# Kernel optimization log

Hardware: AMD Instinct MI355X
Metric: run time of the kernel (lower is better)

The kernel has to match this reference:

```python
import jax, jax.numpy as jnp
import numpy as np

SIZES = [64, 64, 64, 64]
N_SAMPLES = 8192


def radialkernel(u, v):
    # exp(u.v^T - |u|^2/2 - |v|^2/2), shape [rows(u), rows(v)]
    uu = jnp.sum(u * u, axis=1, keepdims=True)
    vv = jnp.sum(v * v, axis=1, keepdims=True)
    return jnp.exp(u @ v.T - uu / 2 - vv.T / 2)


def setup_inputs() -> dict:
    key = jax.random.key(0)
    k0, k1, k2, k3 = jax.random.split(key, 4)
    d_in = 256
    total = sum(SIZES)            # 256
    rest = sum(SIZES[1:])         # 192
    data = jax.random.normal(k0, (N_SAMPLES, d_in), jnp.float32)
    inputs = jax.random.normal(k1, (2048, d_in), jnp.float32)
    # Linear(d_in, total): weight [total, d_in], bias [total]
    W = jax.random.normal(k2, (total, d_in), jnp.float32) / np.sqrt(d_in)
    b = jnp.zeros((total,), jnp.float32)
    # xavier_uniform for c_ss [N, rest]
    limit = np.sqrt(6.0 / (N_SAMPLES + rest)).astype(np.float32)
    c_ss = jax.random.uniform(k3, (N_SAMPLES, rest), jnp.float32, -limit, limit)
    return {"data": data, "inputs": inputs, "W": W, "b": b, "c_ss": c_ss}


def reference(data, inputs, W, b, c_ss):
    n = N_SAMPLES
    x = jnp.concatenate([data, inputs], axis=0) @ W.T + b  # [N+B, total]
    reg = jnp.sum(W * W) + jnp.sum(b * b)
    xss = list(jnp.split(x, np.cumsum(SIZES[:-1]), axis=1))
    css = jnp.split(c_ss, np.cumsum(SIZES[1:-1]), axis=1)
    ker = jnp.zeros((x.shape[0], n), x.dtype)
    for i, cs in enumerate(css):  # len(sizes)-1 iterations (small, fixed)
        xs = xss[i]
        ker = ker + radialkernel(xs, xs[:n])  # [N+B, N]
        val = ker @ cs                        # [N+B, sizes[i+1]]
        xss[i + 1] = xss[i + 1] + val
        reg = reg + jnp.sum(cs * val[:n])
    return xss[-1][n:], reg
```

## Files before the change

kernel.cpp:

```cpp
#include <hip/hip_runtime.h>
#include <hip/hip_bf16.h>

typedef unsigned short u16;
typedef unsigned int   u32;
typedef __attribute__((ext_vector_type(8)))  short bf16x8;
typedef __attribute__((ext_vector_type(16))) float f32x16;

#define N_S   8192
#define M_TOT 10240
#define SEGS  8
#define SEG   1024
#define QT    320

__device__ __forceinline__ u16 f2bf(float f) {
  u32 x = __float_as_uint(f);
  u32 r = x + 0x7FFFu + ((x >> 16) & 1u);
  return (u16)(r >> 16);
}
__device__ __forceinline__ float bf2f(u16 h) {
  return __uint_as_float(((u32)h) << 16);
}

__global__ __launch_bounds__(256) void gemm_x(const float* __restrict__ data,
                                              const float* __restrict__ inp,
                                              const float* __restrict__ W,
                                              const float* __restrict__ bias,
                                              float* __restrict__ x,
                                              u16* __restrict__ xb0,
                                              u32* __restrict__ hl0)
{
  __shared__ __align__(16) u16 At[64 * 256];
  __shared__ __align__(16) u16 Wt[64 * 256];
  __shared__ float part[64][2];
  const int t  = threadIdx.x;
  const int rb = blockIdx.x * 64, cb = blockIdx.y * 64;
  if (cb == 192 && rb + 64 <= N_S) return;

#pragma unroll
  for (int it = 0; it < 8; ++it) {
    int c = it * 256 + t;
    int row = c >> 5, c8 = c & 31;
    int grow = rb + row;
    const float* src = (grow < N_S) ? data + (size_t)grow * 256 + c8 * 8
                                    : inp + (size_t)(grow - N_S) * 256 + c8 * 8;
    float4 v0 = *(const float4*)src;
    float4 v1 = *(const float4*)(src + 4);
    u16 h[8] = {f2bf(v0.x), f2bf(v0.y), f2bf(v0.z), f2bf(v0.w),
                f2bf(v1.x), f2bf(v1.y), f2bf(v1.z), f2bf(v1.w)};
    *(int4*)((char*)At + row * 512 + ((c8 * 16) ^ ((row & 7) << 4))) = *(int4*)h;

    const float* wsrc = W + (size_t)(cb + row) * 256 + c8 * 8;
    float4 w0 = *(const float4*)wsrc;
    float4 w1 = *(const float4*)(wsrc + 4);
    u16 g[8] = {f2bf(w0.x), f2bf(w0.y), f2bf(w0.z), f2bf(w0.w),
                f2bf(w1.x), f2bf(w1.y), f2bf(w1.z), f2bf(w1.w)};
    *(int4*)((char*)Wt + row * 512 + ((c8 * 16) ^ ((row & 7) << 4))) = *(int4*)g;
  }
  __syncthreads();

  const int w = t >> 6, lane = t & 63, l31 = lane & 31, hi = lane >> 5;
  const int wr = (w >> 1) * 32, wc = (w & 1) * 32;
  f32x16 acc;
#pragma unroll
  for (int r = 0; r < 16; ++r) acc[r] = 0.f;
  const char* Ab = (const char*)At + (size_t)(wr + l31) * 512;
  const char* Bb = (const char*)Wt + (size_t)(wc + l31) * 512;
  const int rx = (l31 & 7) << 4;
#pragma unroll
  for (int k0 = 0; k0 < 256; k0 += 16) {
    bf16x8 af = *(const bf16x8*)(Ab + ((k0 * 2 + hi * 16) ^ rx));
    bf16x8 bfv = *(const bf16x8*)(Bb + ((k0 * 2 + hi * 16) ^ rx));
    acc = __builtin_amdgcn_mfma_f32_32x32x16_bf16(af, bfv, acc, 0, 0, 0);
  }
  float bv = bias[cb + wc + l31];
#pragma unroll
  for (int r = 0; r < 16; ++r) {
    int qr = (r & 3) + 8 * (r >> 2) + 4 * hi;
    x[(size_t)(rb + wr + qr) * 256 + cb + wc + l31] = acc[r] + bv;
  }

  if (cb == 0) {
#pragma unroll
    for (int r = 0; r < 16; ++r) {
      int qr = (r & 3) + 8 * (r >> 2) + 4 * hi;
      u16 h = f2bf(acc[r] + bv);
      xb0[(size_t)(rb + wr + qr) * 64 + wc + l31] = h;
      float fb = bf2f(h);
      float s = fb * fb;
      s += __shfl_xor(s, 1);
      s += __shfl_xor(s, 2);
      s += __shfl_xor(s, 4);
      s += __shfl_xor(s, 8);
      s += __shfl_xor(s, 16);
      if (l31 == 0) part[wr + qr][w & 1] = s;
    }
    __syncthreads();
    if (t < 64) {
      float A = 0.5f * (part[t][0] + part[t][1]);
      u16 hq = f2bf(A);
      u16 lq = f2bf(A - bf2f(hq));
      hl0[rb + t] = (u32)hq | ((u32)lq << 16);
    }
  }
}

__global__ __launch_bounds__(256) void setup_ker(const float* __restrict__ css,
                                                 const float* __restrict__ W,
                                                 const float* __restrict__ bias,
                                                 u16* __restrict__ csbT,
                                                 float* __restrict__ regpart,
                                                 u32* __restrict__ mask,
                                                 u32* __restrict__ counter)
{
  __shared__ float tile[64][65];
  __shared__ float red[256];
  const int b = blockIdx.x, t = threadIdx.x;
  if (b < 384) {
    const int i  = b >> 7;
    const int r0 = (b & 127) * 64;
#pragma unroll
    for (int it = 0; it < 4; ++it) {
      int r  = (t >> 4) + it * 16;
      int c4 = (t & 15) * 4;
      float4 v = *(const float4*)(css + (size_t)(r0 + r) * 192 + i * 64 + c4);
      tile[r][c4] = v.x; tile[r][c4 + 1] = v.y; tile[r][c4 + 2] = v.z; tile[r][c4 + 3] = v.w;
    }
    __syncthreads();
    const int c = t >> 2, rq = (t & 3) * 16;
    u16 tmp[16];
#pragma unroll
    for (int e = 0; e < 16; ++e) tmp[e] = f2bf(tile[rq + e][c]);
    u16* dst = csbT + (size_t)i * (64 * (size_t)N_S) + (size_t)c * N_S + r0 + rq;
    *(int4*)dst       = *(int4*)tmp;
    *(int4*)(dst + 8) = *(int4*)(tmp + 8);
  } else {
    const int b2 = b - 384;
    const int gid = b2 * 256 + t;
    if (gid < 3 * QT * SEGS) mask[gid] = 0u;
    if (gid == 0) *counter = 0u;
    float4 v = *(const float4*)(W + (size_t)b2 * 1024 + t * 4);
    float s = v.x * v.x + v.y * v.y + v.z * v.z + v.w * v.w;
    if (b2 == 0) { float bv = bias[t]; s += bv * bv; }
    red[t] = s; __syncthreads();
#pragma unroll
    for (int o = 128; o; o >>= 1) {
      if (t < o) red[t] += red[t + o];
      __syncthreads();
    }
    if (t == 0) regpart[b2] = red[0];
  }
}

__global__ __launch_bounds__(64) void screen_ker(const u16* __restrict__ xbj,
                                                 const u32* __restrict__ hlj,
                                                 u32* __restrict__ maskj)
{
  const int qq  = blockIdx.x;
  const int seg = blockIdx.y;
  const int w   = blockIdx.z;
  const int nt0 = seg * 32 + w * 4;
  if (qq < 64 && qq * 4 + 3 < nt0) return;

  const int lane = threadIdx.x & 63, l31 = lane & 31, hi = lane >> 5;

  bf16x8 qf[4][4];
  u32 hlq[4];
#pragma unroll
  for (int q = 0; q < 4; ++q) {
    const int qrow = (qq * 4 + q) * 32 + l31;
    const u16* qp = xbj + (size_t)qrow * 64 + hi * 8;
#pragma unroll
    for (int d = 0; d < 4; ++d) qf[q][d] = *(const bf16x8*)(qp + d * 16);
    hlq[q] = hlj[qrow];
  }

  f32x16 Z;
#pragma unroll
  for (int r = 0; r < 16; ++r) Z[r] = 0.f;

  u32 bits[4] = {0u, 0u, 0u, 0u};
#pragma unroll
  for (int it = 0; it < 4; ++it) {
    const int kt = nt0 + it;
    const int nb = kt * 32;
    const u16* kp = xbj + (size_t)(nb + l31) * 64 + hi * 8;
    bf16x8 kf0 = *(const bf16x8*)(kp);
    bf16x8 kf1 = *(const bf16x8*)(kp + 16);
    bf16x8 kf2 = *(const bf16x8*)(kp + 32);
    bf16x8 kf3 = *(const bf16x8*)(kp + 48);
    u32 hlk = hlj[nb + l31];
    union { bf16x8 v; u32 d[4]; } ke;
    ke.d[0] = hi ? 0u : 0xBF80BF80u;
    ke.d[1] = hi ? 0u : (hlk ^ 0x80008000u);
    ke.d[2] = 0u; ke.d[3] = 0u;
#pragma unroll
    for (int q = 0; q < 4; ++q) {
      f32x16 S = __builtin_amdgcn_mfma_f32_32x32x16_bf16(qf[q][0], kf0, Z, 0, 0, 0);
      S = __builtin_amdgcn_mfma_f32_32x32x16_bf16(qf[q][1], kf1, S, 0, 0, 0);
      S = __builtin_amdgcn_mfma_f32_32x32x16_bf16(qf[q][2], kf2, S, 0, 0, 0);
      S = __builtin_amdgcn_mfma_f32_32x32x16_bf16(qf[q][3], kf3, S, 0, 0, 0);
      union { bf16x8 v; u32 d[4]; } qe;
      qe.d[0] = hi ? 0u : hlq[q];
      qe.d[1] = hi ? 0u : 0x3F803F80u;
      qe.d[2] = 0u; qe.d[3] = 0u;
      S = __builtin_amdgcn_mfma_f32_32x32x16_bf16(qe.v, ke.v, S, 0, 0, 0);
      float m0 = fmaxf(S[0], S[1]),  m1 = fmaxf(S[2], S[3]);
      float m2 = fmaxf(S[4], S[5]),  m3 = fmaxf(S[6], S[7]);
      float m4 = fmaxf(S[8], S[9]),  m5 = fmaxf(S[10], S[11]);
      float m6 = fmaxf(S[12], S[13]), m7 = fmaxf(S[14], S[15]);
      float mx = fmaxf(fmaxf(fmaxf(m0, m1), fmaxf(m2, m3)),
                       fmaxf(fmaxf(m4, m5), fmaxf(m6, m7)));
      bool act = __any(mx > -25.0f) != 0;
      bits[q] |= (act ? 1u : 0u) << it;
      const int qtile = qq * 4 + q;
      if (act && qtile < 256 && kt < qtile && lane == 0)
        atomicOr(&maskj[(size_t)kt * SEGS + (qtile >> 5)], 1u << (qtile & 31));
    }
  }
  if (lane == 0) {
#pragma unroll
    for (int q = 0; q < 4; ++q)
      if (bits[q]) atomicOr(&maskj[(size_t)(qq * 4 + q) * SEGS + seg], bits[q] << (w * 4));
  }
}

template<int NJ>
__global__ __launch_bounds__(256) void fa_ker(const u16* __restrict__ xb,
                                              const u32* __restrict__ hl,
                                              const u16* __restrict__ csbT,
                                              const u32* __restrict__ mask,
                                              const float* __restrict__ css,
                                              float* __restrict__ x,
                                              float* __restrict__ dotpart,
                                              u16* __restrict__ xbn,
                                              u32* __restrict__ hln,
                                              float* __restrict__ out,
                                              const float* __restrict__ regpart,
                                              u32* __restrict__ counter)
{
  __shared__ __align__(16) u16 Pt[4][32 * 32];
  __shared__ float accs[4][32][64];
  __shared__ float red[256];
  __shared__ int lastFlag;

  const int t    = threadIdx.x;
  const int w    = t >> 6;
  const int lane = t & 63;
  const int l31  = lane & 31;
  const int hi   = lane >> 5;
  const int qtile = blockIdx.x;
  const int qrow  = qtile * 32 + l31;
  constexpr int I = NJ - 1;

  bf16x8 qf[NJ][4];
  u32    hlq[NJ];
#pragma unroll
  for (int j = 0; j < NJ; ++j) {
    const u16* xbj = xb + (size_t)j * ((size_t)M_TOT * 64);
#pragma unroll
    for (int dk = 0; dk < 4; ++dk)
      qf[j][dk] = *(const bf16x8*)(xbj + (size_t)qrow * 64 + dk * 16 + hi * 8);
    hlq[j] = hl[j * M_TOT + qrow];
  }

  f32x16 acc0, acc1;
#pragma unroll
  for (int r = 0; r < 16; ++r) { acc0[r] = 0.f; acc1[r] = 0.f; }

  int idx = 0;
  for (int seg = 0; seg < SEGS; ++seg) {
    u32 mj[NJ];
    u32 uni = 0;
#pragma unroll
    for (int j = 0; j < NJ; ++j) {
      mj[j] = mask[((size_t)j * QT + qtile) * SEGS + seg];
      uni |= mj[j];
    }
    u32 rem = uni;
    while (rem) {
      const int nt = __ffs(rem) - 1;
      rem &= rem - 1;
      if ((idx++ & 3) != w) continue;
      const int nb = seg * SEG + nt * 32;
      f32x16 P;
#pragma unroll
      for (int r = 0; r < 16; ++r) P[r] = 0.f;
#pragma unroll
      for (int j = 0; j < NJ; ++j) {
        if ((mj[j] >> nt) & 1u) {
          const u16* xbj = xb + (size_t)j * ((size_t)M_TOT * 64);
          const u16* kp = xbj + (size_t)(nb + l31) * 64 + hi * 8;
          bf16x8 kf0 = *(const bf16x8*)(kp);
          bf16x8 kf1 = *(const bf16x8*)(kp + 16);
          bf16x8 kf2 = *(const bf16x8*)(kp + 32);
          bf16x8 kf3 = *(const bf16x8*)(kp + 48);
          u32 hlk = hl[j * M_TOT + nb + l31];
          f32x16 S;
#pragma unroll
          for (int r = 0; r < 16; ++r) S[r] = 0.f;
          S = __builtin_amdgcn_mfma_f32_32x32x16_bf16(qf[j][0], kf0, S, 0, 0, 0);
          S = __builtin_amdgcn_mfma_f32_32x32x16_bf16(qf[j][1], kf1, S, 0, 0, 0);
          S = __builtin_amdgcn_mfma_f32_32x32x16_bf16(qf[j][2], kf2, S, 0, 0, 0);
          S = __builtin_amdgcn_mfma_f32_32x32x16_bf16(qf[j][3], kf3, S, 0, 0, 0);
          union { bf16x8 v; u32 d[4]; } qe, ke;
          qe.d[0] = hi ? 0u : hlq[j];
          qe.d[1] = hi ? 0u : 0x3F803F80u;
          qe.d[2] = 0u; qe.d[3] = 0u;
          ke.d[0] = hi ? 0u : 0xBF80BF80u;
          ke.d[1] = hi ? 0u : (hlk ^ 0x80008000u);
          ke.d[2] = 0u; ke.d[3] = 0u;
          S = __builtin_amdgcn_mfma_f32_32x32x16_bf16(qe.v, ke.v, S, 0, 0, 0);
#pragma unroll
          for (int r = 0; r < 16; ++r) P[r] += __expf(S[r]);
        }
      }
      char* pw = (char*)&Pt[w][0];
#pragma unroll
      for (int r = 0; r < 16; ++r) {
        int qr = (r & 3) + 8 * (r >> 2) + 4 * hi;
        *(u16*)(pw + qr * 64 + ((l31 * 2) ^ ((qr & 3) << 4))) = f2bf(P[r]);
      }
      asm volatile("s_waitcnt lgkmcnt(0)" ::: "memory");
      bf16x8 pa0 = *(const bf16x8*)(pw + l31 * 64 + ((0  + hi * 16) ^ ((l31 & 3) << 4)));
      bf16x8 pa1 = *(const bf16x8*)(pw + l31 * 64 + ((32 + hi * 16) ^ ((l31 & 3) << 4)));
      asm volatile("s_waitcnt lgkmcnt(0)" ::: "memory");
      bf16x8 v00 = *(const bf16x8*)(csbT + (size_t)l31 * N_S + nb + hi * 8);
      bf16x8 v01 = *(const bf16x8*)(csbT + (size_t)l31 * N_S + nb + 16 + hi * 8);
      bf16x8 v10 = *(const bf16x8*)(csbT + (size_t)(32 + l31) * N_S + nb + hi * 8);
      bf16x8 v11 = *(const bf16x8*)(csbT + (size_t)(32 + l31) * N_S + nb + 16 + hi * 8);
      acc0 = __builtin_amdgcn_mfma_f32_32x32x16_bf16(pa0, v00, acc0, 0, 0, 0);
      acc0 = __builtin_amdgcn_mfma_f32_32x32x16_bf16(pa1, v01, acc0, 0, 0, 0);
      acc1 = __builtin_amdgcn_mfma_f32_32x32x16_bf16(pa0, v10, acc1, 0, 0, 0);
      acc1 = __builtin_amdgcn_mfma_f32_32x32x16_bf16(pa1, v11, acc1, 0, 0, 0);
    }
  }

#pragma unroll
  for (int r = 0; r < 16; ++r) {
    int qr = (r & 3) + 8 * (r >> 2) + 4 * hi;
    accs[w][qr][l31]      = acc0[r];
    accs[w][qr][32 + l31] = acc1[r];
  }
  __syncthreads();

  const int rr   = t >> 3;
  const int row  = qtile * 32 + rr;
  const int coff = (t & 7) * 8;
  float v[8];
#pragma unroll
  for (int e = 0; e < 8; ++e)
    v[e] = ((accs[0][rr][coff + e] + accs[1][rr][coff + e]) +
            (accs[2][rr][coff + e] + accs[3][rr][coff + e]));

  float dp = 0.f;
  if (row < N_S) {
    const float* cp = css + (size_t)row * 192 + (size_t)I * 64 + coff;
    float4 ca = *(const float4*)cp;
    float4 cb = *(const float4*)(cp + 4);
    dp = ca.x * v[0] + ca.y * v[1] + ca.z * v[2] + ca.w * v[3]
       + cb.x * v[4] + cb.y * v[5] + cb.z * v[6] + cb.w * v[7];
  }

  if (NJ < 3) {
    float* xp = x + (size_t)row * 256 + (size_t)(I + 1) * 64 + coff;
    float4 xa = *(const float4*)xp;
    float4 xb4 = *(const float4*)(xp + 4);
    xa.x += v[0]; xa.y += v[1]; xa.z += v[2]; xa.w += v[3];
    xb4.x += v[4]; xb4.y += v[5]; xb4.z += v[6]; xb4.w += v[7];
    *(float4*)xp = xa;
    *(float4*)(xp + 4) = xb4;
    float xv[8] = {xa.x, xa.y, xa.z, xa.w, xb4.x, xb4.y, xb4.z, xb4.w};
    u16 h[8];
    float s2 = 0.f;
#pragma unroll
    for (int e = 0; e < 8; ++e) {
      h[e] = f2bf(xv[e]);
      float fb = bf2f(h[e]);
      s2 += fb * fb;
    }
    *(int4*)(xbn + (size_t)row * 64 + coff) = *(int4*)h;
    s2 += __shfl_xor(s2, 1);
    s2 += __shfl_xor(s2, 2);
    s2 += __shfl_xor(s2, 4);
    if ((t & 7) == 0) {
      float A = 0.5f * s2;
      u16 hq = f2bf(A);
      u16 lq = f2bf(A - bf2f(hq));
      hln[row] = (u32)hq | ((u32)lq << 16);
    }
  } else if (row >= N_S) {
    const float* xp = x + (size_t)row * 256 + 192 + coff;
    float4 xa = *(const float4*)xp;
    float4 xb4 = *(const float4*)(xp + 4);
    float* op = out + (size_t)(row - N_S) * 64 + coff;
    float4 oa = {xa.x + v[0], xa.y + v[1], xa.z + v[2], xa.w + v[3]};
    float4 ob = {xb4.x + v[4], xb4.y + v[5], xb4.z + v[6], xb4.w + v[7]};
    *(float4*)op = oa;
    *(float4*)(op + 4) = ob;
  }

  red[t] = dp; __syncthreads();
#pragma unroll
  for (int o = 128; o; o >>= 1) {
    if (t < o) red[t] += red[t + o];
    __syncthreads();
  }
  if (t == 0) dotpart[I * QT + qtile] = red[0];

  if (NJ == 3) {
    if (t == 0) {
      u32 c = __hip_atomic_fetch_add(counter, 1u, __ATOMIC_ACQ_REL, __HIP_MEMORY_SCOPE_AGENT);
      lastFlag = (c == QT - 1) ? 1 : 0;
    }
    __syncthreads();
    if (lastFlag) {
      float s = 0.f;
      for (int i2 = t; i2 < 3 * QT; i2 += 256) s += dotpart[i2];
      if (t < 64) s += regpart[t];
      red[t] = s; __syncthreads();
#pragma unroll
      for (int o = 128; o; o >>= 1) {
        if (t < o) red[t] += red[t + o];
        __syncthreads();
      }
      if (t == 0) out[131072] = red[0];
    }
  }
}

extern "C" void kernel_launch(void* const* d_in, const int* in_sizes, int n_in,
                              void* d_out, int out_size, void* d_ws, size_t ws_size,
                              hipStream_t stream)
{
  const float* data = (const float*)d_in[0];
  const float* inp  = (const float*)d_in[1];
  const float* W    = (const float*)d_in[2];
  const float* bias = (const float*)d_in[3];
  const float* css  = (const float*)d_in[4];
  float* out = (float*)d_out;

  char* ws = (char*)d_ws;
  const size_t OFF_X    = 0;
  const size_t OFF_XB   = 10485760;
  const size_t OFF_HL   = OFF_XB + 3932160;
  const size_t OFF_CSBT = OFF_HL + 122880;
  const size_t OFF_MASK = OFF_CSBT + 3145728;
  const size_t OFF_REGW = OFF_MASK + 30720;
  const size_t OFF_DOT  = OFF_REGW + 256;
  const size_t OFF_CNT  = OFF_DOT + 3840;

  float* x      = (float*)(ws + OFF_X);
  u16*   xb     = (u16*)  (ws + OFF_XB);
  u32*   hl     = (u32*)  (ws + OFF_HL);
  u16*   csbT   = (u16*)  (ws + OFF_CSBT);
  u32*   mask   = (u32*)  (ws + OFF_MASK);
  float* regpart= (float*)(ws + OFF_REGW);
  float* dotpart= (float*)(ws + OFF_DOT);
  u32*   counter= (u32*)  (ws + OFF_CNT);

  const size_t XB_STRIDE = (size_t)M_TOT * 64;
  const size_t CS_STRIDE = (size_t)64 * N_S;
  const size_t MK_STRIDE = (size_t)QT * SEGS;

  setup_ker<<<448, 256, 0, stream>>>(css, W, bias, csbT, regpart, mask, counter);
  gemm_x   <<<dim3(160, 4), 256, 0, stream>>>(data, inp, W, bias, x, xb, hl);
  screen_ker<<<dim3(80, SEGS, 8), 64, 0, stream>>>(xb, hl, mask);

  fa_ker<1><<<QT, 256, 0, stream>>>(xb, hl, csbT, mask, css, x, dotpart,
                                    xb + XB_STRIDE, hl + M_TOT, (float*)nullptr,
                                    regpart, counter);
  screen_ker<<<dim3(80, SEGS, 8), 64, 0, stream>>>(xb + XB_STRIDE, hl + M_TOT, mask + MK_STRIDE);

  fa_ker<2><<<QT, 256, 0, stream>>>(xb, hl, csbT + CS_STRIDE, mask, css, x, dotpart,
                                    xb + 2 * XB_STRIDE, hl + 2 * M_TOT, (float*)nullptr,
                                    regpart, counter);
  screen_ker<<<dim3(80, SEGS, 8), 64, 0, stream>>>(xb + 2 * XB_STRIDE, hl + 2 * M_TOT, mask + 2 * MK_STRIDE);

  fa_ker<3><<<QT, 256, 0, stream>>>(xb, hl, csbT + 2 * CS_STRIDE, mask, css, x, dotpart,
                                    (u16*)nullptr, (u32*)nullptr, out,
                                    regpart, counter);
}
```

Baseline: 134.5 us.

## Fuse setup into projection GEMM and skip empty query tiles in attention

Merges the setup kernel (transposing c_ss to bf16, zeroing the mask, reducing the weight norms) into the projection GEMM as extra blocks, so one launch replaces two. The GEMM now also writes the bf16 copy and half-norms for column blocks 1 and 2. This lets each fa_ker block whose screening masks are all empty skip the query loads, the kernel accumulation and the x/xbn update entirely. The cost is a larger shared-memory footprint per GEMM block and extra bf16 stores that run even for tiles that do real work.

```diff
diff --git a/kernel.cpp b/kernel.cpp
--- a/kernel.cpp
+++ b/kernel.cpp
@@ -21,20 +21,70 @@
   return __uint_as_float(((u32)h) << 16);
 }
 
-__global__ __launch_bounds__(256) void gemm_x(const float* __restrict__ data,
-                                              const float* __restrict__ inp,
-                                              const float* __restrict__ W,
-                                              const float* __restrict__ bias,
-                                              float* __restrict__ x,
-                                              u16* __restrict__ xb0,
-                                              u32* __restrict__ hl0)
+__global__ __launch_bounds__(256) void gemm_setup(const float* __restrict__ data,
+                                                  const float* __restrict__ inp,
+                                                  const float* __restrict__ W,
+                                                  const float* __restrict__ bias,
+                                                  const float* __restrict__ css,
+                                                  float* __restrict__ x,
+                                                  u16* __restrict__ xb,
+                                                  u32* __restrict__ hl,
+                                                  u16* __restrict__ csbT,
+                                                  float* __restrict__ regpart,
+                                                  u32* __restrict__ mask,
+                                                  u32* __restrict__ counter)
 {
-  __shared__ __align__(16) u16 At[64 * 256];
-  __shared__ __align__(16) u16 Wt[64 * 256];
-  __shared__ float part[64][2];
-  const int t  = threadIdx.x;
-  const int rb = blockIdx.x * 64, cb = blockIdx.y * 64;
+  __shared__ __align__(16) char smem[66048];
+  const int b = blockIdx.x, t = threadIdx.x;
+
+  if (b >= 640) {
+    const int bs = b - 640;
+    if (bs < 384) {
+      float (*tile)[65] = (float(*)[65])smem;
+      const int i  = bs >> 7;
+      const int r0 = (bs & 127) * 64;
+#pragma unroll
+      for (int it = 0; it < 4; ++it) {
+        int r  = (t >> 4) + it * 16;
+        int c4 = (t & 15) * 4;
+        float4 v = *(const float4*)(css + (size_t)(r0 + r) * 192 + i * 64 + c4);
+        tile[r][c4] = v.x; tile[r][c4 + 1] = v.y; tile[r][c4 + 2] = v.z; tile[r][c4 + 3] = v.w;
+      }
+      __syncthreads();
+      const int c = t >> 2, rq = (t & 3) * 16;
+      u16 tmp[16];
+#pragma unroll
+      for (int e = 0; e < 16; ++e) tmp[e] = f2bf(tile[rq + e][c]);
+      u16* dst = csbT + (size_t)i * (64 * (size_t)N_S) + (size_t)c * N_S + r0 + rq;
+      *(int4*)dst       = *(int4*)tmp;
+      *(int4*)(dst + 8) = *(int4*)(tmp + 8);
+    } else {
+      float* red = (float*)smem;
+      const int b2 = bs - 384;
+      const int gid = b2 * 256 + t;
+      if (gid < 3 * QT * SEGS) mask[gid] = 0u;
+      if (gid == 0) *counter = 0u;
+      float4 v = *(const float4*)(W + (size_t)b2 * 1024 + t * 4);
+      float s = v.x * v.x + v.y * v.y + v.z * v.z + v.w * v.w;
+      if (b2 == 0) { float bv = bias[t]; s += bv * bv; }
+      red[t] = s; __syncthreads();
+#pragma unroll
+      for (int o = 128; o; o >>= 1) {
+        if (t < o) red[t] += red[t + o];
+        __syncthreads();
+      }
+      if (t == 0) regpart[b2] = red[0];
+    }
+    return;
+  }
+
+  const int rowblk = b >> 2, cbi = b & 3;
+  const int rb = rowblk * 64, cb = cbi * 64;
   if (cb == 192 && rb + 64 <= N_S) return;
+
+  u16* At = (u16*)smem;
+  u16* Wt = (u16*)(smem + 32768);
+  float (*part)[2] = (float(*)[2])(smem + 65536);
 
 #pragma unroll
   for (int it = 0; it < 8; ++it) {
@@ -79,12 +129,14 @@
     x[(size_t)(rb + wr + qr) * 256 + cb + wc + l31] = acc[r] + bv;
   }
 
-  if (cb == 0) {
+  if (cb < 192) {
+    u16* xbc = xb + (size_t)cbi * ((size_t)M_TOT * 64);
+    u32* hlc = hl + (size_t)cbi * M_TOT;
 #pragma unroll
     for (int r = 0; r < 16; ++r) {
       int qr = (r & 3) + 8 * (r >> 2) + 4 * hi;
       u16 h = f2bf(acc[r] + bv);
-      xb0[(size_t)(rb + wr + qr) * 64 + wc + l31] = h;
+      xbc[(size_t)(rb + wr + qr) * 64 + wc + l31] = h;
       float fb = bf2f(h);
       float s = fb * fb;
       s += __shfl_xor(s, 1);
@@ -99,55 +151,8 @@
       float A = 0.5f * (part[t][0] + part[t][1]);
       u16 hq = f2bf(A);
       u16 lq = f2bf(A - bf2f(hq));
-      hl0[rb + t] = (u32)hq | ((u32)lq << 16);
-    }
-  }
-}
-
-__global__ __launch_bounds__(256) void setup_ker(const float* __restrict__ css,
-                                                 const float* __restrict__ W,
-                                                 const float* __restrict__ bias,
-                                                 u16* __restrict__ csbT,
-                                                 float* __restrict__ regpart,
-                                                 u32* __restrict__ mask,
-                                                 u32* __restrict__ counter)
-{
-  __shared__ float tile[64][65];
-  __shared__ float red[256];
-  const int b = blockIdx.x, t = threadIdx.x;
-  if (b < 384) {
-    const int i  = b >> 7;
-    const int r0 = (b & 127) * 64;
-#pragma unroll
-    for (int it = 0; it < 4; ++it) {
-      int r  = (t >> 4) + it * 16;
-      int c4 = (t & 15) * 4;
-      float4 v = *(const float4*)(css + (size_t)(r0 + r) * 192 + i * 64 + c4);
-      tile[r][c4] = v.x; tile[r][c4 + 1] = v.y; tile[r][c4 + 2] = v.z; tile[r][c4 + 3] = v.w;
-    }
-    __syncthreads();
-    const int c = t >> 2, rq = (t & 3) * 16;
-    u16 tmp[16];
-#pragma unroll
-    for (int e = 0; e < 16; ++e) tmp[e] = f2bf(tile[rq + e][c]);
-    u16* dst = csbT + (size_t)i * (64 * (size_t)N_S) + (size_t)c * N_S + r0 + rq;
-    *(int4*)dst       = *(int4*)tmp;
-    *(int4*)(dst + 8) = *(int4*)(tmp + 8);
-  } else {
-    const int b2 = b - 384;
-    const int gid = b2 * 256 + t;
-    if (gid < 3 * QT * SEGS) mask[gid] = 0u;
-    if (gid == 0) *counter = 0u;
-    float4 v = *(const float4*)(W + (size_t)b2 * 1024 + t * 4);
-    float s = v.x * v.x + v.y * v.y + v.z * v.z + v.w * v.w;
-    if (b2 == 0) { float bv = bias[t]; s += bv * bv; }
-    red[t] = s; __syncthreads();
-#pragma unroll
-    for (int o = 128; o; o >>= 1) {
-      if (t < o) red[t] += red[t + o];
-      __syncthreads();
-    }
-    if (t == 0) regpart[b2] = red[0];
+      hlc[rb + t] = (u32)hq | ((u32)lq << 16);
+    }
   }
 }
 
@@ -252,141 +257,157 @@
   const int qrow  = qtile * 32 + l31;
   constexpr int I = NJ - 1;
 
-  bf16x8 qf[NJ][4];
-  u32    hlq[NJ];
-#pragma unroll
-  for (int j = 0; j < NJ; ++j) {
-    const u16* xbj = xb + (size_t)j * ((size_t)M_TOT * 64);
-#pragma unroll
-    for (int dk = 0; dk < 4; ++dk)
-      qf[j][dk] = *(const bf16x8*)(xbj + (size_t)qrow * 64 + dk * 16 + hi * 8);
-    hlq[j] = hl[j * M_TOT + qrow];
-  }
-
-  f32x16 acc0, acc1;
-#pragma unroll
-  for (int r = 0; r < 16; ++r) { acc0[r] = 0.f; acc1[r] = 0.f; }
-
-  int idx = 0;
+  u32 mj_all[NJ][SEGS];
+  u32 uni_s[SEGS];
+  u32 anyu = 0;
+#pragma unroll
   for (int seg = 0; seg < SEGS; ++seg) {
-    u32 mj[NJ];
-    u32 uni = 0;
+    u32 u = 0;
 #pragma unroll
     for (int j = 0; j < NJ; ++j) {
-      mj[j] = mask[((size_t)j * QT + qtile) * SEGS + seg];
-      uni |= mj[j];
-    }
-    u32 rem = uni;
-    while (rem) {
-      const int nt = __ffs(rem) - 1;
-      rem &= rem - 1;
-      if ((idx++ & 3) != w) continue;
-      const int nb = seg * SEG + nt * 32;
-      f32x16 P;
-#pragma unroll
-      for (int r = 0; r < 16; ++r) P[r] = 0.f;
-#pragma unroll
-      for (int j = 0; j < NJ; ++j) {
-        if ((mj[j] >> nt) & 1u) {
-          const u16* xbj = xb + (size_t)j * ((size_t)M_TOT * 64);
-          const u16* kp = xbj + (size_t)(nb + l31) * 64 + hi * 8;
-          bf16x8 kf0 = *(const bf16x8*)(kp);
-          bf16x8 kf1 = *(const bf16x8*)(kp + 16);
-          bf16x8 kf2 = *(const bf16x8*)(kp + 32);
-          bf16x8 kf3 = *(const bf16x8*)(kp + 48);
-          u32 hlk = hl[j * M_TOT + nb + l31];
-          f32x16 S;
-#pragma unroll
-          for (int r = 0; r < 16; ++r) S[r] = 0.f;
-          S = __builtin_amdgcn_mfma_f32_32x32x16_bf16(qf[j][0], kf0, S, 0, 0, 0);
-          S = __builtin_amdgcn_mfma_f32_32x32x16_bf16(qf[j][1], kf1, S, 0, 0, 0);
-          S = __builtin_amdgcn_mfma_f32_32x32x16_bf16(qf[j][2], kf2, S, 0, 0, 0);
-          S = __builtin_amdgcn_mfma_f32_32x32x16_bf16(qf[j][3], kf3, S, 0, 0, 0);
-          union { bf16x8 v; u32 d[4]; } qe, ke;
-          qe.d[0] = hi ? 0u : hlq[j];
-          qe.d[1] = hi ? 0u : 0x3F803F80u;
-          qe.d[2] = 0u; qe.d[3] = 0u;
-          ke.d[0] = hi ? 0u : 0xBF80BF80u;
-          ke.d[1] = hi ? 0u : (hlk ^ 0x80008000u);
-          ke.d[2] = 0u; ke.d[3] = 0u;
-          S = __builtin_amdgcn_mfma_f32_32x32x16_bf16(qe.v, ke.v, S, 0, 0, 0);
-#pragma unroll
-          for (int r = 0; r < 16; ++r) P[r] += __expf(S[r]);
+      mj_all[j][seg] = mask[((size_t)j * QT + qtile) * SEGS + seg];
+      u |= mj_all[j][seg];
+    }
+    uni_s[seg] = u;
+    anyu |= u;
+  }
+
+  if (anyu) {
+    bf16x8 qf[NJ][4];
+    u32    hlq[NJ];
+#pragma unroll
+    for (int j = 0; j < NJ; ++j) {
+      const u16* xbj = xb + (size_t)j * ((size_t)M_TOT * 64);
+#pragma unroll
+      for (int dk = 0; dk < 4; ++dk)
+        qf[j][dk] = *(const bf16x8*)(xbj + (size_t)qrow * 64 + dk * 16 + hi * 8);
+      hlq[j] = hl[j * M_TOT + qrow];
+    }
+
+    f32x16 acc0, acc1;
+#pragma unroll
+    for (int r = 0; r < 16; ++r) { acc0[r] = 0.f; acc1[r] = 0.f; }
+
+    int idx = 0;
+    for (int seg = 0; seg < SEGS; ++seg) {
+      u32 rem = uni_s[seg];
+      while (rem) {
+        const int nt = __ffs(rem) - 1;
+        rem &= rem - 1;
+        if ((idx++ & 3) != w) continue;
+        const int nb = seg * SEG + nt * 32;
+        f32x16 P;
+#pragma unroll
+        for (int r = 0; r < 16; ++r) P[r] = 0.f;
+#pragma unroll
+        for (int j = 0; j < NJ; ++j) {
+          if ((mj_all[j][seg] >> nt) & 1u) {
+            const u16* xbj = xb + (size_t)j * ((size_t)M_TOT * 64);
+            const u16* kp = xbj + (size_t)(nb + l31) * 64 + hi * 8;
+            bf16x8 kf0 = *(const bf16x8*)(kp);
+            bf16x8 kf1 = *(const bf16x8*)(kp + 16);
+            bf16x8 kf2 = *(const bf16x8*)(kp + 32);
+            bf16x8 kf3 = *(const bf16x8*)(kp + 48);
+            u32 hlk = hl[j * M_TOT + nb + l31];
+            f32x16 S;
+#pragma unroll
+            for (int r = 0; r < 16; ++r) S[r] = 0.f;
+            S = __builtin_amdgcn_mfma_f32_32x32x16_bf16(qf[j][0], kf0, S, 0, 0, 0);
+            S = __builtin_amdgcn_mfma_f32_32x32x16_bf16(qf[j][1], kf1, S, 0, 0, 0);
+            S = __builtin_amdgcn_mfma_f32_32x32x16_bf16(qf[j][2], kf2, S, 0, 0, 0);
+            S = __builtin_amdgcn_mfma_f32_32x32x16_bf16(qf[j][3], kf3, S, 0, 0, 0);
+            union { bf16x8 v; u32 d[4]; } qe, ke;
+            qe.d[0] = hi ? 0u : hlq[j];
+            qe.d[1] = hi ? 0u : 0x3F803F80u;
+            qe.d[2] = 0u; qe.d[3] = 0u;
+            ke.d[0] = hi ? 0u : 0xBF80BF80u;
+            ke.d[1] = hi ? 0u : (hlk ^ 0x80008000u);
+            ke.d[2] = 0u; ke.d[3] = 0u;
+            S = __builtin_amdgcn_mfma_f32_32x32x16_bf16(qe.v, ke.v, S, 0, 0, 0);
+#pragma unroll
+            for (int r = 0; r < 16; ++r) P[r] += __expf(S[r]);
+          }
         }
+        char* pw = (char*)&Pt[w][0];
+#pragma unroll
+        for (int r = 0; r < 16; ++r) {
+          int qr = (r & 3) + 8 * (r >> 2) + 4 * hi;
+          *(u16*)(pw + qr * 64 + ((l31 * 2) ^ ((qr & 3) << 4))) = f2bf(P[r]);
+        }
+        asm volatile("s_waitcnt lgkmcnt(0)" ::: "memory");
+        bf16x8 pa0 = *(const bf16x8*)(pw + l31 * 64 + ((0  + hi * 16) ^ ((l31 & 3) << 4)));
+        bf16x8 pa1 = *(const bf16x8*)(pw + l31 * 64 + ((32 + hi * 16) ^ ((l31 & 3) << 4)));
+        asm volatile("s_waitcnt lgkmcnt(0)" ::: "memory");
+        bf16x8 v00 = *(const bf16x8*)(csbT + (size_t)l31 * N_S + nb + hi * 8);
+        bf16x8 v01 = *(const bf16x8*)(csbT + (size_t)l31 * N_S + nb + 16 + hi * 8);
+        bf16x8 v10 = *(const bf16x8*)(csbT + (size_t)(32 + l31) * N_S + nb + hi * 8);
+        bf16x8 v11 = *(const bf16x8*)(csbT + (size_t)(32 + l31) * N_S + nb + 16 + hi * 8);
+        acc0 = __builtin_amdgcn_mfma_f32_32x32x16_bf16(pa0, v00, acc0, 0, 0, 0);
+        acc0 = __builtin_amdgcn_mfma_f32_32x32x16_bf16(pa1, v01, acc0, 0, 0, 0);
+        acc1 = __builtin_amdgcn_mfma_f32_32x32x16_bf16(pa0, v10, acc1, 0, 0, 0);
+        acc1 = __builtin_amdgcn_mfma_f32_32x32x16_bf16(pa1, v11, acc1, 0, 0, 0);
       }
-      char* pw = (char*)&Pt[w][0];
-#pragma unroll
-      for (int r = 0; r < 16; ++r) {
-        int qr = (r & 3) + 8 * (r >> 2) + 4 * hi;
-        *(u16*)(pw + qr * 64 + ((l31 * 2) ^ ((qr & 3) << 4))) = f2bf(P[r]);
-      }
-      asm volatile("s_waitcnt lgkmcnt(0)" ::: "memory");
-      bf16x8 pa0 = *(const bf16x8*)(pw + l31 * 64 + ((0  + hi * 16) ^ ((l31 & 3) << 4)));
-      bf16x8 pa1 = *(const bf16x8*)(pw + l31 * 64 + ((32 + hi * 16) ^ ((l31 & 3) << 4)));
-      asm volatile("s_waitcnt lgkmcnt(0)" ::: "memory");
-      bf16x8 v00 = *(const bf16x8*)(csbT + (size_t)l31 * N_S + nb + hi * 8);
-      bf16x8 v01 = *(const bf16x8*)(csbT + (size_t)l31 * N_S + nb + 16 + hi * 8);
-      bf16x8 v10 = *(const bf16x8*)(csbT + (size_t)(32 + l31) * N_S + nb + hi * 8);
-      bf16x8 v11 = *(const bf16x8*)(csbT + (size_t)(32 + l31) * N_S + nb + 16 + hi * 8);
-      acc0 = __builtin_amdgcn_mfma_f32_32x32x16_bf16(pa0, v00, acc0, 0, 0, 0);
-      acc0 = __builtin_amdgcn_mfma_f32_32x32x16_bf16(pa1, v01, acc0, 0, 0, 0);
-      acc1 = __builtin_amdgcn_mfma_f32_32x32x16_bf16(pa0, v10, acc1, 0, 0, 0);
-      acc1 = __builtin_amdgcn_mfma_f32_32x32x16_bf16(pa1, v11, acc1, 0, 0, 0);
-    }
-  }
-
-#pragma unroll
-  for (int r = 0; r < 16; ++r) {
-    int qr = (r & 3) + 8 * (r >> 2) + 4 * hi;
-    accs[w][qr][l31]      = acc0[r];
-    accs[w][qr][32 + l31] = acc1[r];
-  }
-  __syncthreads();
+    }
+
+#pragma unroll
+    for (int r = 0; r < 16; ++r) {
+      int qr = (r & 3) + 8 * (r >> 2) + 4 * hi;
+      accs[w][qr][l31]      = acc0[r];
+      accs[w][qr][32 + l31] = acc1[r];
+    }
+    __syncthreads();
+  }
 
   const int rr   = t >> 3;
   const int row  = qtile * 32 + rr;
   const int coff = (t & 7) * 8;
   float v[8];
 #pragma unroll
-  for (int e = 0; e < 8; ++e)
-    v[e] = ((accs[0][rr][coff + e] + accs[1][rr][coff + e]) +
-            (accs[2][rr][coff + e] + accs[3][rr][coff + e]));
-
+  for (int e = 0; e < 8; ++e) v[e] = 0.f;
   float dp = 0.f;
-  if (row < N_S) {
-    const float* cp = css + (size_t)row * 192 + (size_t)I * 64 + coff;
-    float4 ca = *(const float4*)cp;
-    float4 cb = *(const float4*)(cp + 4);
-    dp = ca.x * v[0] + ca.y * v[1] + ca.z * v[2] + ca.w * v[3]
-       + cb.x * v[4] + cb.y * v[5] + cb.z * v[6] + cb.w * v[7];
+
+  if (anyu) {
+#pragma unroll
+    for (int e = 0; e < 8; ++e)
+      v[e] = ((accs[0][rr][coff + e] + accs[1][rr][coff + e]) +
+              (accs[2][rr][coff + e] + accs[3][rr][coff + e]));
+    if (row < N_S) {
+      const float* cp = css + (size_t)row * 192 + (size_t)I * 64 + coff;
+      float4 ca = *(const float4*)cp;
+      float4 cb = *(const float4*)(cp + 4);
+      dp = ca.x * v[0] + ca.y * v[1] + ca.z * v[2] + ca.w * v[3]
+         + cb.x * v[4] + cb.y * v[5] + cb.z * v[6] + cb.w * v[7];
+    }
   }
 
   if (NJ < 3) {
-    float* xp = x + (size_t)row * 256 + (size_t)(I + 1) * 64 + coff;
-    float4 xa = *(const float4*)xp;
-    float4 xb4 = *(const float4*)(xp + 4);
-    xa.x += v[0]; xa.y += v[1]; xa.z += v[2]; xa.w += v[3];
-    xb4.x += v[4]; xb4.y += v[5]; xb4.z += v[6]; xb4.w += v[7];
-    *(float4*)xp = xa;
-    *(float4*)(xp + 4) = xb4;
-    float xv[8] = {xa.x, xa.y, xa.z, xa.w, xb4.x, xb4.y, xb4.z, xb4.w};
-    u16 h[8];
-    float s2 = 0.f;
-#pragma unroll
-    for (int e = 0; e < 8; ++e) {
-      h[e] = f2bf(xv[e]);
-      float fb = bf2f(h[e]);
-      s2 += fb * fb;
-    }
-    *(int4*)(xbn + (size_t)row * 64 + coff) = *(int4*)h;
-    s2 += __shfl_xor(s2, 1);
-    s2 += __shfl_xor(s2, 2);
-    s2 += __shfl_xor(s2, 4);
-    if ((t & 7) == 0) {
-      float A = 0.5f * s2;
-      u16 hq = f2bf(A);
-      u16 lq = f2bf(A - bf2f(hq));
-      hln[row] = (u32)hq | ((u32)lq << 16);
+    if (anyu) {
+      float* xp = x + (size_t)row * 256 + (size_t)(I + 1) * 64 + coff;
+      float4 xa = *(const float4*)xp;
+      float4 xb4 = *(const float4*)(xp + 4);
+      xa.x += v[0]; xa.y += v[1]; xa.z += v[2]; xa.w += v[3];
+      xb4.x += v[4]; xb4.y += v[5]; xb4.z += v[6]; xb4.w += v[7];
+      *(float4*)xp = xa;
+      *(float4*)(xp + 4) = xb4;
+      float xv[8] = {xa.x, xa.y, xa.z, xa.w, xb4.x, xb4.y, xb4.z, xb4.w};
+      u16 h[8];
+      float s2 = 0.f;
+#pragma unroll
+      for (int e = 0; e < 8; ++e) {
+        h[e] = f2bf(xv[e]);
+        float fb = bf2f(h[e]);
+        s2 += fb * fb;
+      }
+      *(int4*)(xbn + (size_t)row * 64 + coff) = *(int4*)h;
+      s2 += __shfl_xor(s2, 1);
+      s2 += __shfl_xor(s2, 2);
+      s2 += __shfl_xor(s2, 4);
+      if ((t & 7) == 0) {
+        float A = 0.5f * s2;
+        u16 hq = f2bf(A);
+        u16 lq = f2bf(A - bf2f(hq));
+        hln[row] = (u32)hq | ((u32)lq << 16);
+      }
     }
   } else if (row >= N_S) {
     const float* xp = x + (size_t)row * 256 + 192 + coff;
@@ -462,8 +483,8 @@
   const size_t CS_STRIDE = (size_t)64 * N_S;
   const size_t MK_STRIDE = (size_t)QT * SEGS;
 
-  setup_ker<<<448, 256, 0, stream>>>(css, W, bias, csbT, regpart, mask, counter);
-  gemm_x   <<<dim3(160, 4), 256, 0, stream>>>(data, inp, W, bias, x, xb, hl);
+  gemm_setup<<<1088, 256, 0, stream>>>(data, inp, W, bias, css, x, xb, hl,
+                                       csbT, regpart, mask, counter);
   screen_ker<<<dim3(80, SEGS, 8), 64, 0, stream>>>(xb, hl, mask);
 
   fa_ker<1><<<QT, 256, 0, stream>>>(xb, hl, csbT, mask, css, x, dotpart,
```

After: 140.1 us. 4.2% more time.
